# Kernel tuning notes

Hardware: AMD Instinct MI355X
Metric: run time of the kernel (lower is better)

Reference implementation:

```python
import jax, jax.numpy as jnp
import numpy as np

B, C, H, W = 32, 256, 56, 56
G, K, RED = 2, 7, 4
BN_EPS = 1e-5


def _conv2d(x, w, pad, groups=1, bias=None):
    # x: (N, Cin, H, W), w: (Cout, Cin/groups, kh, kw)
    y = jax.lax.conv_general_dilated(
        x, w, window_strides=(1, 1), padding=[(pad, pad), (pad, pad)],
        dimension_numbers=("NCHW", "OIHW", "NCHW"), feature_group_count=groups)
    if bias is not None:
        y = y + bias[None, :, None, None]
    return y


def setup_inputs() -> dict:
    key = jax.random.key(0)
    ks = jax.random.split(key, 5)
    return {
        "x": jax.random.normal(ks[0], (B, C, H, W), jnp.float32),
        "w_dyn": jax.random.normal(ks[1], (G, C, K, K), jnp.float32) * 0.02,
        "proj1_w": jax.random.normal(ks[2], (C // RED, C, 3, 3), jnp.float32) * 0.02,
        "bn_gamma": jnp.ones((C // RED,), jnp.float32),
        "bn_beta": jnp.zeros((C // RED,), jnp.float32),
        "proj2_w": jax.random.normal(ks[3], (C * G, C // RED, 3, 3), jnp.float32) * 0.02,
        "proj2_b": jnp.zeros((C * G,), jnp.float32),
    }


def reference(x, w_dyn, proj1_w, bn_gamma, bn_beta, proj2_w, proj2_b):
    b, c, h, w = x.shape
    # AdaptiveAvgPool2d((K, K)); H, W divisible by K -> exact mean over (H//K, W//K) windows
    pooled = x.reshape(b, c, K, h // K, K, w // K).mean(axis=(3, 5))  # (B, C, K, K)
    # proj: Conv3x3 (no bias, BN follows) -> BN (inference: mean=0, var=1) -> GELU -> Conv3x3
    hmid = _conv2d(pooled, proj1_w, pad=1)
    hmid = hmid * (bn_gamma / jnp.sqrt(1.0 + BN_EPS))[None, :, None, None] + bn_beta[None, :, None, None]
    hmid = jax.nn.gelu(hmid, approximate=False)
    scale = _conv2d(hmid, proj2_w, pad=1, bias=proj2_b)  # (B, G*C, K, K)
    scale = jax.nn.softmax(scale.reshape(b, G, c, K, K), axis=1)
    # per-sample dynamic depthwise kernel: softmax-weighted mix of G kernel banks
    dyn_w = jnp.einsum("bgckl,gckl->bckl", scale, w_dyn)  # (B, C, K, K)
    # depthwise conv with per-sample weights: groups = B*C
    y = _conv2d(x.reshape(1, b * c, h, w), dyn_w.reshape(b * c, 1, K, K),
                pad=K // 2, groups=b * c)
    return y.reshape(b, c, h, w)
```

## Files before the change

kernel.cpp:

```cpp
#include <hip/hip_runtime.h>
#include <math.h>

#define BB 32
#define CC 256
#define HH 56
#define WW 56
#define KP 49
#define CMID 64
#define HW 3136

#define RSTR 64
#define PROWS 62
#define PSZ (PROWS * RSTR)

__global__ __launch_bounds__(256) void transpose_w_kernel(const float* __restrict__ w1,
                                                          const float* __restrict__ w2,
                                                          float* __restrict__ w1t,
                                                          float* __restrict__ w2t) {
    int tid = blockIdx.x * 256 + threadIdx.x;
    if (tid < 147456) {
        int co = tid & 63, ct = tid >> 6;
        w1t[tid] = w1[co * 2304 + ct];
    }
    if (tid < 294912) {
        int co = tid & 511, ct = tid >> 9;
        w2t[tid] = w2[co * 576 + ct];
    }
}

__global__ __launch_bounds__(256) void pool_kernel(const float* __restrict__ x,
                                                   float* __restrict__ pooled) {
    int wv = threadIdx.x >> 6, lane = threadIdx.x & 63;
    int g = blockIdx.x * 4 + wv;
    if (lane < KP) {
        int ko = lane / 7, kw = lane - ko * 7;
        const float* base = x + (size_t)g * HW + (ko * 8) * WW + kw * 8;
        float s = 0.f;
        #pragma unroll
        for (int r = 0; r < 8; ++r) {
            float4 a = *(const float4*)(base + r * WW);
            float4 b4 = *(const float4*)(base + r * WW + 4);
            s += a.x + a.y + a.z + a.w + b4.x + b4.y + b4.z + b4.w;
        }
        pooled[(size_t)g * KP + lane] = s * (1.f / 64.f);
    }
}

__global__ __launch_bounds__(512) void conv1_kernel(const float* __restrict__ pooled,
                                                    const float* __restrict__ w1t,
                                                    const float* __restrict__ gamma,
                                                    const float* __restrict__ beta,
                                                    float* __restrict__ hmid) {
    int y = blockIdx.x, b = blockIdx.y;
    int wv = threadIdx.x >> 6, co = threadIdx.x & 63;
    __shared__ float red[8][7][64];
    float acc[7] = {0.f, 0.f, 0.f, 0.f, 0.f, 0.f, 0.f};
    const float* pb = pooled + (size_t)b * CC * KP;
    for (int ci = 0; ci < 32; ++ci) {
        int cin = wv * 32 + ci;
        const float* prow_base = pb + cin * KP;
        const float* wbase = w1t + (size_t)(cin * 9) * 64 + co;
        #pragma unroll
        for (int ky = 0; ky < 3; ++ky) {
            int iy = y + ky - 1;
            if (0 <= iy && iy < 7) {
                float s[9];
                s[0] = 0.f; s[8] = 0.f;
                const float* pr = prow_base + iy * 7;
                #pragma unroll
                for (int j = 0; j < 7; ++j) s[j + 1] = pr[j];
                const float* wr = wbase + ky * 3 * 64;
                float w0 = wr[0], w1v = wr[64], w2v = wr[128];
                #pragma unroll
                for (int xx = 0; xx < 7; ++xx)
                    acc[xx] += s[xx] * w0 + s[xx + 1] * w1v + s[xx + 2] * w2v;
            }
        }
    }
    #pragma unroll
    for (int xx = 0; xx < 7; ++xx) red[wv][xx][co] = acc[xx];
    __syncthreads();
    if (threadIdx.x < 448) {
        int xx = threadIdx.x >> 6, c2 = threadIdx.x & 63;
        float tot = 0.f;
        #pragma unroll
        for (int w = 0; w < 8; ++w) tot += red[w][xx][c2];
        float bnscale = gamma[c2] * rsqrtf(1.f + 1e-5f);
        float h = tot * bnscale + beta[c2];
        float g = 0.5f * h * (1.f + erff(h * 0.70710678118654752440f));
        hmid[((size_t)b * CMID + c2) * KP + y * 7 + xx] = g;
    }
}

__global__ __launch_bounds__(512) void conv2_kernel(const float* __restrict__ hmid,
                                                    const float* __restrict__ w2t,
                                                    const float* __restrict__ b2,
                                                    const float* __restrict__ wdyn,
                                                    float* __restrict__ dynw) {
    int y = blockIdx.x, b = blockIdx.y;
    int g = threadIdx.x >> 8, co = threadIdx.x & 255;
    __shared__ float redA[2][7][256];
    __shared__ float redB[2][7][256];
    float a0[7] = {}, a1[7] = {};
    const float* hb = hmid + (size_t)b * CMID * KP;
    for (int ci = 0; ci < 32; ++ci) {
        int cin = g * 32 + ci;
        const float* hrow_base = hb + cin * KP;
        const float* wbase = w2t + (size_t)(cin * 9) * 512 + co;
        #pragma unroll
        for (int ky = 0; ky < 3; ++ky) {
            int iy = y + ky - 1;
            if (0 <= iy && iy < 7) {
                float s[9];
                s[0] = 0.f; s[8] = 0.f;
                const float* hr = hrow_base + iy * 7;
                #pragma unroll
                for (int j = 0; j < 7; ++j) s[j + 1] = hr[j];
                const float* wr = wbase + ky * 3 * 512;
                float wa0 = wr[0],    wb0 = wr[256];
                float wa1 = wr[512],  wb1 = wr[768];
                float wa2 = wr[1024], wb2 = wr[1280];
                #pragma unroll
                for (int xx = 0; xx < 7; ++xx) {
                    float v0 = s[xx], v1 = s[xx + 1], v2 = s[xx + 2];
                    a0[xx] += v0 * wa0 + v1 * wa1 + v2 * wa2;
                    a1[xx] += v0 * wb0 + v1 * wb1 + v2 * wb2;
                }
            }
        }
    }
    #pragma unroll
    for (int xx = 0; xx < 7; ++xx) { redA[g][xx][co] = a0[xx]; redB[g][xx][co] = a1[xx]; }
    __syncthreads();
    if (threadIdx.x < 256) {
        int c = threadIdx.x;
        float bias0 = b2[c], bias1 = b2[c + CC];
        const float* wd0 = wdyn + (size_t)c * KP + y * 7;
        const float* wd1 = wdyn + (size_t)(CC + c) * KP + y * 7;
        float* dw = dynw + ((size_t)(b * CC + c)) * KP + y * 7;
        #pragma unroll
        for (int xx = 0; xx < 7; ++xx) {
            float s0 = redA[0][xx][c] + redA[1][xx][c] + bias0;
            float s1 = redB[0][xx][c] + redB[1][xx][c] + bias1;
            float m = fmaxf(s0, s1);
            float e0 = expf(s0 - m), e1 = expf(s1 - m);
            dw[xx] = (e0 * wd0[xx] + e1 * wd1[xx]) / (e0 + e1);
        }
    }
}

__global__ __launch_bounds__(256) void dwconv_kernel(const float* __restrict__ x,
                                                     const float* __restrict__ dynw,
                                                     float* __restrict__ out) {
    __shared__ float xs[4 * PSZ];
    int tid = threadIdx.x;
    int g0 = blockIdx.x * 4;

    float4* xs4 = (float4*)xs;
    for (int e = tid; e < 4 * PSZ / 4; e += 256)
        xs4[e] = make_float4(0.f, 0.f, 0.f, 0.f);
    __syncthreads();

    for (int idx = tid; idx < 4 * 56 * 14; idx += 256) {
        int p   = idx / 784;
        int rem = idx - p * 784;
        int r   = rem / 14;
        int c4  = rem - r * 14;
        float4 v = *((const float4*)(x + ((size_t)(g0 + p)) * HW + r * WW) + c4);
        int pr    = r + 3;
        int shift = 4 * ((pr >> 3) & 7);
        int col   = (4 * c4 + 4 + shift) & 63;
        *(float4*)(xs + p * PSZ + pr * RSTR + col) = v;
    }
    __syncthreads();

    int wv = tid >> 6, lane = tid & 63;
    int gplane = __builtin_amdgcn_readfirstlane(g0 + wv);
    const float* wp = dynw + (size_t)gplane * KP;
    float w[49];
    #pragma unroll
    for (int i = 0; i < 49; ++i) w[i] = wp[i];

    if (lane < KP) {
        int ty = lane / 7, tx = lane - ty * 7;
        int r0 = 8 * ty, c0 = 8 * tx;
        const float* pbase = xs + wv * PSZ;
        float acc[8][8] = {};
        #pragma unroll
        for (int ir = 0; ir < 14; ++ir) {
            int pr = r0 + ir;
            int shift = 4 * ((pr >> 3) & 7);
            const float* rowp = pbase + pr * RSTR;
            float rb[16];
            #pragma unroll
            for (int k = 0; k < 4; ++k) {
                int col = (c0 + shift + 4 * k) & 63;
                float4 v = *(const float4*)(rowp + col);
                rb[4 * k + 0] = v.x; rb[4 * k + 1] = v.y;
                rb[4 * k + 2] = v.z; rb[4 * k + 3] = v.w;
            }
            #pragma unroll
            for (int ky = 0; ky < 7; ++ky) {
                int oy = ir - ky;
                if (0 <= oy && oy < 8) {
                    #pragma unroll
                    for (int kx = 0; kx < 7; ++kx) {
                        float ww = w[ky * 7 + kx];
                        #pragma unroll
                        for (int ox = 0; ox < 8; ++ox)
                            acc[oy][ox] += rb[ox + 1 + kx] * ww;
                    }
                }
            }
        }
        float* op = out + (size_t)(g0 + wv) * HW;
        #pragma unroll
        for (int oy = 0; oy < 8; ++oy) {
            float* orow = op + (r0 + oy) * WW + c0;
            *(float4*)(orow)     = make_float4(acc[oy][0], acc[oy][1], acc[oy][2], acc[oy][3]);
            *(float4*)(orow + 4) = make_float4(acc[oy][4], acc[oy][5], acc[oy][6], acc[oy][7]);
        }
    }
}

extern "C" void kernel_launch(void* const* d_in, const int* in_sizes, int n_in,
                              void* d_out, int out_size, void* d_ws, size_t ws_size,
                              hipStream_t stream) {
    const float* x     = (const float*)d_in[0];
    const float* wdyn  = (const float*)d_in[1];
    const float* w1    = (const float*)d_in[2];
    const float* gamma = (const float*)d_in[3];
    const float* beta  = (const float*)d_in[4];
    const float* w2    = (const float*)d_in[5];
    const float* b2    = (const float*)d_in[6];
    float* out = (float*)d_out;

    float* ws     = (float*)d_ws;
    float* pooled = ws;
    float* hmid   = ws + 401408;
    float* dynw   = ws + 501760;
    float* w1t    = ws + 903168;
    float* w2t    = ws + 1050624;

    transpose_w_kernel<<<dim3(1152),        256, 0, stream>>>(w1, w2, w1t, w2t);
    pool_kernel       <<<dim3(BB * CC / 4), 256, 0, stream>>>(x, pooled);
    conv1_kernel      <<<dim3(7, BB),       512, 0, stream>>>(pooled, w1t, gamma, beta, hmid);
    conv2_kernel      <<<dim3(7, BB),       512, 0, stream>>>(hmid, w2t, b2, wdyn, dynw);
    dwconv_kernel     <<<dim3(BB * CC / 4), 256, 0, stream>>>(x, dynw, out);
}
```

Before: 322.3 us.

## Split conv1/conv2 input channels across blocks and rewrite dwconv with shuffles

Conv1 and conv2 now split their input-channel reduction over a grid z dimension, writing partial sums that separate epilogue kernels add up before applying BN+GELU or the softmax mix. This raises block count for these small convs, at the cost of extra launches and partial-sum traffic. The depthwise conv drops the shared-memory padded tile and uses one block per plane, with one lane per column and a wave per 8 rows. Horizontal neighbours now come from wave shuffles, removing LDS staging and barriers, but each wave rereads its 6 halo rows from global memory.

```diff
diff --git a/kernel.cpp b/kernel.cpp
--- a/kernel.cpp
+++ b/kernel.cpp
@@ -8,10 +8,6 @@
 #define KP 49
 #define CMID 64
 #define HW 3136
-
-#define RSTR 64
-#define PROWS 62
-#define PSZ (PROWS * RSTR)
 
 __global__ __launch_bounds__(256) void transpose_w_kernel(const float* __restrict__ w1,
                                                           const float* __restrict__ w2,
@@ -46,18 +42,18 @@
     }
 }
 
-__global__ __launch_bounds__(512) void conv1_kernel(const float* __restrict__ pooled,
-                                                    const float* __restrict__ w1t,
-                                                    const float* __restrict__ gamma,
-                                                    const float* __restrict__ beta,
-                                                    float* __restrict__ hmid) {
-    int y = blockIdx.x, b = blockIdx.y;
-    int wv = threadIdx.x >> 6, co = threadIdx.x & 63;
+__global__ __launch_bounds__(512) void conv1_part_kernel(const float* __restrict__ pooled,
+                                                         const float* __restrict__ w1t,
+                                                         float* __restrict__ p1) {
+    int y = blockIdx.x, b = blockIdx.y, z = blockIdx.z;
+    int wvu = __builtin_amdgcn_readfirstlane(threadIdx.x >> 6);
+    int co = threadIdx.x & 63;
     __shared__ float red[8][7][64];
     float acc[7] = {0.f, 0.f, 0.f, 0.f, 0.f, 0.f, 0.f};
     const float* pb = pooled + (size_t)b * CC * KP;
-    for (int ci = 0; ci < 32; ++ci) {
-        int cin = wv * 32 + ci;
+    #pragma unroll 2
+    for (int ci = 0; ci < 8; ++ci) {
+        int cin = z * 64 + wvu * 8 + ci;
         const float* prow_base = pb + cin * KP;
         const float* wbase = w1t + (size_t)(cin * 9) * 64 + co;
         #pragma unroll
@@ -78,33 +74,46 @@
         }
     }
     #pragma unroll
-    for (int xx = 0; xx < 7; ++xx) red[wv][xx][co] = acc[xx];
+    for (int xx = 0; xx < 7; ++xx) red[wvu][xx][co] = acc[xx];
     __syncthreads();
     if (threadIdx.x < 448) {
         int xx = threadIdx.x >> 6, c2 = threadIdx.x & 63;
         float tot = 0.f;
         #pragma unroll
         for (int w = 0; w < 8; ++w) tot += red[w][xx][c2];
-        float bnscale = gamma[c2] * rsqrtf(1.f + 1e-5f);
-        float h = tot * bnscale + beta[c2];
+        p1[(size_t)z * 100352 + ((size_t)(b * CMID + c2)) * KP + y * 7 + xx] = tot;
+    }
+}
+
+__global__ __launch_bounds__(256) void conv1_epi_kernel(const float* __restrict__ p1,
+                                                        const float* __restrict__ gamma,
+                                                        const float* __restrict__ beta,
+                                                        float* __restrict__ hmid) {
+    int idx = blockIdx.x * 256 + threadIdx.x;
+    if (idx < 100352) {
+        float tot = p1[idx] + p1[idx + 100352] + p1[idx + 200704] + p1[idx + 301056];
+        int co = (idx / KP) & 63;
+        float bnscale = gamma[co] * rsqrtf(1.f + 1e-5f);
+        float h = tot * bnscale + beta[co];
         float g = 0.5f * h * (1.f + erff(h * 0.70710678118654752440f));
-        hmid[((size_t)b * CMID + c2) * KP + y * 7 + xx] = g;
-    }
-}
-
-__global__ __launch_bounds__(512) void conv2_kernel(const float* __restrict__ hmid,
-                                                    const float* __restrict__ w2t,
-                                                    const float* __restrict__ b2,
-                                                    const float* __restrict__ wdyn,
-                                                    float* __restrict__ dynw) {
-    int y = blockIdx.x, b = blockIdx.y;
-    int g = threadIdx.x >> 8, co = threadIdx.x & 255;
+        hmid[idx] = g;
+    }
+}
+
+__global__ __launch_bounds__(512) void conv2_part_kernel(const float* __restrict__ hmid,
+                                                         const float* __restrict__ w2t,
+                                                         float* __restrict__ pA,
+                                                         float* __restrict__ pB) {
+    int y = blockIdx.x, b = blockIdx.y, z = blockIdx.z;
+    int gu = __builtin_amdgcn_readfirstlane(threadIdx.x >> 8);
+    int co = threadIdx.x & 255;
     __shared__ float redA[2][7][256];
     __shared__ float redB[2][7][256];
     float a0[7] = {}, a1[7] = {};
     const float* hb = hmid + (size_t)b * CMID * KP;
-    for (int ci = 0; ci < 32; ++ci) {
-        int cin = g * 32 + ci;
+    #pragma unroll 2
+    for (int ci = 0; ci < 16; ++ci) {
+        int cin = z * 32 + gu * 16 + ci;
         const float* hrow_base = hb + cin * KP;
         const float* wbase = w2t + (size_t)(cin * 9) * 512 + co;
         #pragma unroll
@@ -130,96 +139,80 @@
         }
     }
     #pragma unroll
-    for (int xx = 0; xx < 7; ++xx) { redA[g][xx][co] = a0[xx]; redB[g][xx][co] = a1[xx]; }
+    for (int xx = 0; xx < 7; ++xx) { redA[gu][xx][co] = a0[xx]; redB[gu][xx][co] = a1[xx]; }
     __syncthreads();
     if (threadIdx.x < 256) {
         int c = threadIdx.x;
-        float bias0 = b2[c], bias1 = b2[c + CC];
-        const float* wd0 = wdyn + (size_t)c * KP + y * 7;
-        const float* wd1 = wdyn + (size_t)(CC + c) * KP + y * 7;
-        float* dw = dynw + ((size_t)(b * CC + c)) * KP + y * 7;
+        size_t base = (size_t)z * 401408 + ((size_t)(b * CC + c)) * KP + y * 7;
         #pragma unroll
         for (int xx = 0; xx < 7; ++xx) {
-            float s0 = redA[0][xx][c] + redA[1][xx][c] + bias0;
-            float s1 = redB[0][xx][c] + redB[1][xx][c] + bias1;
-            float m = fmaxf(s0, s1);
-            float e0 = expf(s0 - m), e1 = expf(s1 - m);
-            dw[xx] = (e0 * wd0[xx] + e1 * wd1[xx]) / (e0 + e1);
-        }
-    }
-}
-
-__global__ __launch_bounds__(256) void dwconv_kernel(const float* __restrict__ x,
+            pA[base + xx] = redA[0][xx][c] + redA[1][xx][c];
+            pB[base + xx] = redB[0][xx][c] + redB[1][xx][c];
+        }
+    }
+}
+
+__global__ __launch_bounds__(256) void conv2_epi_kernel(const float* __restrict__ pA,
+                                                        const float* __restrict__ pB,
+                                                        const float* __restrict__ b2,
+                                                        const float* __restrict__ wdyn,
+                                                        float* __restrict__ dynw) {
+    int idx = blockIdx.x * 256 + threadIdx.x;
+    if (idx < 401408) {
+        int pix = idx % KP;
+        int c = (idx / KP) & 255;
+        float s0 = pA[idx] + pA[idx + 401408] + b2[c];
+        float s1 = pB[idx] + pB[idx + 401408] + b2[c + CC];
+        float m = fmaxf(s0, s1);
+        float e0 = expf(s0 - m), e1 = expf(s1 - m);
+        float wd0 = wdyn[c * KP + pix];
+        float wd1 = wdyn[(CC + c) * KP + pix];
+        dynw[idx] = (e0 * wd0 + e1 * wd1) / (e0 + e1);
+    }
+}
+
+__global__ __launch_bounds__(448) void dwconv_kernel(const float* __restrict__ x,
                                                      const float* __restrict__ dynw,
                                                      float* __restrict__ out) {
-    __shared__ float xs[4 * PSZ];
-    int tid = threadIdx.x;
-    int g0 = blockIdx.x * 4;
-
-    float4* xs4 = (float4*)xs;
-    for (int e = tid; e < 4 * PSZ / 4; e += 256)
-        xs4[e] = make_float4(0.f, 0.f, 0.f, 0.f);
-    __syncthreads();
-
-    for (int idx = tid; idx < 4 * 56 * 14; idx += 256) {
-        int p   = idx / 784;
-        int rem = idx - p * 784;
-        int r   = rem / 14;
-        int c4  = rem - r * 14;
-        float4 v = *((const float4*)(x + ((size_t)(g0 + p)) * HW + r * WW) + c4);
-        int pr    = r + 3;
-        int shift = 4 * ((pr >> 3) & 7);
-        int col   = (4 * c4 + 4 + shift) & 63;
-        *(float4*)(xs + p * PSZ + pr * RSTR + col) = v;
-    }
-    __syncthreads();
-
-    int wv = tid >> 6, lane = tid & 63;
-    int gplane = __builtin_amdgcn_readfirstlane(g0 + wv);
-    const float* wp = dynw + (size_t)gplane * KP;
+    int plane = blockIdx.x;
+    int wv = threadIdx.x >> 6;
+    int lane = threadIdx.x & 63;
+    const float* wp = dynw + (size_t)plane * KP;
     float w[49];
     #pragma unroll
     for (int i = 0; i < 49; ++i) w[i] = wp[i];
-
-    if (lane < KP) {
-        int ty = lane / 7, tx = lane - ty * 7;
-        int r0 = 8 * ty, c0 = 8 * tx;
-        const float* pbase = xs + wv * PSZ;
-        float acc[8][8] = {};
-        #pragma unroll
-        for (int ir = 0; ir < 14; ++ir) {
-            int pr = r0 + ir;
-            int shift = 4 * ((pr >> 3) & 7);
-            const float* rowp = pbase + pr * RSTR;
-            float rb[16];
-            #pragma unroll
-            for (int k = 0; k < 4; ++k) {
-                int col = (c0 + shift + 4 * k) & 63;
-                float4 v = *(const float4*)(rowp + col);
-                rb[4 * k + 0] = v.x; rb[4 * k + 1] = v.y;
-                rb[4 * k + 2] = v.z; rb[4 * k + 3] = v.w;
+    int r0 = wv << 3;
+    const float* xp = x + (size_t)plane * HW;
+    float* op = out + (size_t)plane * HW;
+    float acc[8] = {};
+    bool active = lane < WW;
+    #pragma unroll
+    for (int i = 0; i < 14; ++i) {
+        int ir = r0 + i - 3;
+        float v = 0.f;
+        if (0 <= ir && ir < HH && active) v = xp[ir * WW + lane];
+        float sh[7];
+        sh[0] = __shfl(v, (lane - 3) & 63);
+        sh[1] = __shfl(v, (lane - 2) & 63);
+        sh[2] = __shfl(v, (lane - 1) & 63);
+        sh[3] = v;
+        sh[4] = __shfl(v, (lane + 1) & 63);
+        sh[5] = __shfl(v, (lane + 2) & 63);
+        sh[6] = __shfl(v, (lane + 3) & 63);
+        #pragma unroll
+        for (int ky = 0; ky < 7; ++ky) {
+            int oy = i - ky;
+            if (0 <= oy && oy < 8) {
+                #pragma unroll
+                for (int kx = 0; kx < 7; ++kx)
+                    acc[oy] += sh[kx] * w[ky * 7 + kx];
             }
-            #pragma unroll
-            for (int ky = 0; ky < 7; ++ky) {
-                int oy = ir - ky;
-                if (0 <= oy && oy < 8) {
-                    #pragma unroll
-                    for (int kx = 0; kx < 7; ++kx) {
-                        float ww = w[ky * 7 + kx];
-                        #pragma unroll
-                        for (int ox = 0; ox < 8; ++ox)
-                            acc[oy][ox] += rb[ox + 1 + kx] * ww;
-                    }
-                }
-            }
-        }
-        float* op = out + (size_t)(g0 + wv) * HW;
-        #pragma unroll
-        for (int oy = 0; oy < 8; ++oy) {
-            float* orow = op + (r0 + oy) * WW + c0;
-            *(float4*)(orow)     = make_float4(acc[oy][0], acc[oy][1], acc[oy][2], acc[oy][3]);
-            *(float4*)(orow + 4) = make_float4(acc[oy][4], acc[oy][5], acc[oy][6], acc[oy][7]);
-        }
+        }
+    }
+    if (active) {
+        #pragma unroll
+        for (int o = 0; o < 8; ++o)
+            op[(r0 + o) * WW + lane] = acc[o];
     }
 }
 
@@ -236,15 +229,20 @@
     float* out = (float*)d_out;
 
     float* ws     = (float*)d_ws;
-    float* pooled = ws;
-    float* hmid   = ws + 401408;
-    float* dynw   = ws + 501760;
-    float* w1t    = ws + 903168;
-    float* w2t    = ws + 1050624;
-
-    transpose_w_kernel<<<dim3(1152),        256, 0, stream>>>(w1, w2, w1t, w2t);
-    pool_kernel       <<<dim3(BB * CC / 4), 256, 0, stream>>>(x, pooled);
-    conv1_kernel      <<<dim3(7, BB),       512, 0, stream>>>(pooled, w1t, gamma, beta, hmid);
-    conv2_kernel      <<<dim3(7, BB),       512, 0, stream>>>(hmid, w2t, b2, wdyn, dynw);
-    dwconv_kernel     <<<dim3(BB * CC / 4), 256, 0, stream>>>(x, dynw, out);
-}
+    float* hmid   = ws;
+    float* dynw   = ws + 100352;
+    float* w1t    = ws + 501760;
+    float* w2t    = ws + 649216;
+    float* pooled = ws + 944128;
+    float* p1     = ws + 1345536;
+    float* pA     = ws + 944128;
+    float* pB     = ws + 1746944;
+
+    transpose_w_kernel<<<dim3(1152),         256, 0, stream>>>(w1, w2, w1t, w2t);
+    pool_kernel       <<<dim3(BB * CC / 4),  256, 0, stream>>>(x, pooled);
+    conv1_part_kernel <<<dim3(7, BB, 4),     512, 0, stream>>>(pooled, w1t, p1);
+    conv1_epi_kernel  <<<dim3(392),          256, 0, stream>>>(p1, gamma, beta, hmid);
+    conv2_part_kernel <<<dim3(7, BB, 2),     512, 0, stream>>>(hmid, w2t, pA, pB);
+    conv2_epi_kernel  <<<dim3(1568),         256, 0, stream>>>(pA, pB, b2, wdyn, dynw);
+    dwconv_kernel     <<<dim3(BB * CC),      448, 0, stream>>>(x, dynw, out);
+}
```

New measurement: 347.1 us. 7.7% more time.
